# Kernel optimization log

Hardware: AMD Instinct MI355X
Metric: run time of the kernel (lower is better)

## Reference

```python
import jax, jax.numpy as jnp
import numpy as np

B = 16384          # scenes (batch_size)
K = 16             # vehicles per scene (1 hero + 15 neighbors)
IN_LEN = 16        # in_length
OUT_LEN = 25       # out_length
ALL_LEN = 41       # all_length
T_H = IN_LEN - 1
ENC = 64           # encoder_size
N = B * K
NN = B * (K - 1)


def setup_inputs() -> dict:
    key = jax.random.key(0)
    ks = jax.random.split(key, 20)
    scene = jax.random.normal(ks[0], (N, 2, ALL_LEN), jnp.float32)
    idx = jnp.arange(N, dtype=jnp.int32)
    hero_index = idx[::K]                 # hero is first vehicle of each group
    nbr_index = idx[idx % K != 0]         # remaining K-1 vehicles, group-major
    w = lambda k, s: jax.random.normal(k, s, jnp.float32) * 0.1
    return {
        'scene': scene, 'hero_index': hero_index, 'nbr_index': nbr_index,
        'W_h1': w(ks[1], (2 * IN_LEN, 32)), 'b_h1': w(ks[2], (32,)),
        'W_h2': w(ks[3], (32, ENC)), 'b_h2': w(ks[4], (ENC,)),
        'W_f1': w(ks[5], (2 * OUT_LEN, 32)), 'b_f1': w(ks[6], (32,)),
        'W_f2': w(ks[7], (32, ENC)), 'b_f2': w(ks[8], (ENC,)),
        'W_dyn': w(ks[9], (ENC, 32)), 'b_dyn': w(ks[10], (32,)),
        'W_nbr': w(ks[11], (2 * IN_LEN, ENC)), 'b_nbr': w(ks[12], (ENC,)),
        'W_out': w(ks[13], (96, 128)), 'b_out': w(ks[14], (128,)),
        'W_op': w(ks[15], (128, 1)), 'b_op': w(ks[16], (1,)),
    }


def reference(scene, hero_index, nbr_index,
              W_h1, b_h1, W_h2, b_h2, W_f1, b_f1, W_f2, b_f2,
              W_dyn, b_dyn, W_nbr, b_nbr, W_out, b_out, W_op, b_op):
    lrelu = lambda x: jax.nn.leaky_relu(x, 0.1)
    # per-scene reference pose = hero position at t_h, broadcast to all vehicles
    ref = scene[hero_index, :, T_H][:, :, None]              # (B,2,1)
    scene = scene - jnp.repeat(ref, K, axis=0)               # (N,2,ALL_LEN)
    # per-scene, per-channel scale = max |history| over vehicles and time
    scale = jnp.abs(scene[:, :, :IN_LEN]).reshape(B, K, 2, IN_LEN).max(axis=(1, 3))  # (B,2)
    scene = scene / jnp.repeat(scale, K, axis=0)[:, :, None]
    hero = scene[hero_index]                                 # (B,2,ALL_LEN)
    nbrs = scene[nbr_index]                                  # (NN,2,ALL_LEN)
    hist = hero[:, :, :IN_LEN].transpose(0, 2, 1)            # (B,IN_LEN,2)
    fut = hero[:, :, IN_LEN:IN_LEN + OUT_LEN].transpose(0, 2, 1)  # (B,OUT_LEN,2)
    nb_hist = nbrs[:, :, :IN_LEN].transpose(0, 2, 1)         # (NN,IN_LEN,2)
    rel = jnp.repeat(hist, K - 1, axis=0) - nb_hist          # (NN,IN_LEN,2)
    hist_f = hist.reshape(B, 2 * IN_LEN)
    fut_f = fut.reshape(B, 2 * OUT_LEN)
    rel_f = rel.reshape(NN, 2 * IN_LEN)
    # hero history encoder (mlp_net) + dyn_emb
    hist_enc = lrelu(lrelu(hist_f @ W_h1 + b_h1) @ W_h2 + b_h2)
    hist_enc = lrelu(hist_enc @ W_dyn + b_dyn)
    # neighbor relative encoder + per-scene max pool + dyn_emb
    rela_enc = lrelu(rel_f @ W_nbr + b_nbr)                  # (NN,ENC)
    pooled = rela_enc.reshape(B, K - 1, ENC).max(axis=1)     # (B,ENC)
    pooled = lrelu(pooled @ W_dyn + b_dyn)
    # future encoder (mlp_net_fut) + dyn_emb
    fut_enc = lrelu(lrelu(fut_f @ W_f1 + b_f1) @ W_f2 + b_f2)
    fut_enc = lrelu(fut_enc @ W_dyn + b_dyn)
    enc = jnp.concatenate([hist_enc, pooled, fut_enc], axis=1)  # (B,96)
    feature_enc = lrelu(enc @ W_out + b_out)                 # (B,128)
    logit = jax.nn.sigmoid(feature_enc @ W_op + b_op)        # (B,1)
    return logit, feature_enc
```

## Files before the change

kernel.cpp:

```cpp
#include <hip/hip_runtime.h>
#include <hip/hip_bf16.h>
#include <math.h>

#define NB 16384

typedef short short8 __attribute__((ext_vector_type(8)));
typedef float f32x4 __attribute__((ext_vector_type(4)));

__device__ __forceinline__ float lrelu(float x){ return x > 0.f ? x : 0.1f*x; }

__device__ __forceinline__ unsigned short f2b(float f){
  unsigned u = __builtin_bit_cast(unsigned, f);
  u = (u + 0x7fffu + ((u >> 16) & 1u)) >> 16;
  return (unsigned short)u;
}

#define MFMA(a,b,c) __builtin_amdgcn_mfma_f32_16x16x32_bf16((a),(b),(c),0,0,0)

__device__ __forceinline__ short8 afrag(const unsigned short* tile, int stride_us, int kbase){
  const int l = threadIdx.x & 63;
  return *(const short8*)(tile + (size_t)(l & 15) * stride_us + kbase + ((l >> 4) * 8));
}

__device__ __forceinline__ short8 ldfrag(const unsigned short* __restrict__ frags, int slot, int idx){
  return *(const short8*)(frags + ((size_t)((slot * 8 + idx) * 64 + (threadIdx.x & 63)) * 8));
}

__global__ __launch_bounds__(64) void prep_frags(
    const float* __restrict__ W_h1, const float* __restrict__ W_f1,
    const float* __restrict__ W_h2, const float* __restrict__ W_f2,
    const float* __restrict__ W_dyn, const float* __restrict__ W_nbr,
    const float* __restrict__ W_out, unsigned short* __restrict__ frags)
{
  const int bid = blockIdx.x;
  const int slot = bid >> 3, w = bid & 7;
  const int l = threadIdx.x;
  const int n16 = l & 15, q = l >> 4;
  short8 r = {0,0,0,0,0,0,0,0};
  #pragma unroll
  for (int e = 0; e < 8; ++e){
    const int p = q * 8 + e;
    int i = -1, n = -1, ldn = 0;
    const float* W = nullptr;
    switch (slot){
      case 0:  W = W_nbr; ldn = 64;  n = (w & 3) * 16 + n16; i = 2*(p&15) + (p>>4); break;
      case 1:  W = W_h1;  ldn = 32;  n = (w & 1) * 16 + n16; i = 2*(p&15) + (p>>4); break;
      case 2:  W = W_f1;  ldn = 32;  n = (w & 1) * 16 + n16; i = (p < 25) ? 2*p   : -1; break;
      case 3:  W = W_f1;  ldn = 32;  n = (w & 1) * 16 + n16; i = (p < 25) ? 2*p+1 : -1; break;
      case 4:  W = W_dyn; ldn = 32;  n = (w & 1) * 16 + n16; i = p;      break;
      case 5:  W = W_dyn; ldn = 32;  n = (w & 1) * 16 + n16; i = 32 + p; break;
      case 6:  W = W_h2;  ldn = 64;  n = (w & 3) * 16 + n16; i = p; break;
      case 7:  W = W_f2;  ldn = 64;  n = (w & 3) * 16 + n16; i = p; break;
      case 8:  W = W_out; ldn = 128; n = w * 16 + n16;       i = p;      break;
      case 9:  W = W_out; ldn = 128; n = w * 16 + n16;       i = 32 + p; break;
      case 10: W = W_out; ldn = 128; n = w * 16 + n16;       i = 64 + p; break;
    }
    const float v = (W && i >= 0) ? W[i * ldn + n] : 0.f;
    r[e] = (short)f2b(v);
  }
  *(short8*)(frags + (size_t)(bid * 64 + l) * 8) = r;
}

__global__ __launch_bounds__(512) void highway_fused(
    const float* __restrict__ scene,
    const unsigned short* __restrict__ frags,
    const float* __restrict__ b_h1, const float* __restrict__ b_h2,
    const float* __restrict__ b_f1, const float* __restrict__ b_f2,
    const float* __restrict__ b_dyn, const float* __restrict__ b_nbr,
    const float* __restrict__ b_out, const float* __restrict__ W_op,
    const float* __restrict__ b_op,
    float* __restrict__ logit, float* __restrict__ feat)
{
  __shared__ __align__(16) unsigned short An[15 * 648];
  __shared__ __align__(16) unsigned short Ah[16][40];
  __shared__ __align__(16) unsigned short Af[16][72];
  __shared__ __align__(16) unsigned short Apool[16][72];
  __shared__ __align__(16) unsigned short As1h[16][40];
  __shared__ __align__(16) unsigned short As1f[16][40];
  __shared__ __align__(16) unsigned short As2h[16][72];
  __shared__ __align__(16) unsigned short As2f[16][72];
  __shared__ __align__(16) unsigned short Aenc[16][104];
  __shared__ float tmpP[4][16][17];
  __shared__ float red[8][16];

  const int tid = threadIdx.x;
  const int w = tid >> 6, l = tid & 63;
  const int g0 = blockIdx.x * 16;

  {
    const int g = tid >> 5, s = tid & 31;
    const int c = s >> 4, t = s & 15;
    const float* sc = scene + (size_t)(g0 + g) * 1312;

    float v[16];
    #pragma unroll
    for (int k = 0; k < 16; ++k) v[k] = sc[k * 82 + c * 41 + t];
    const float vf0 = sc[c * 41 + 16 + t];
    const float vf1 = (t < 9) ? sc[c * 41 + 32 + t] : 0.f;

    const float ref = __shfl(v[0], (l & 32) | (c << 4) | 15, 64);

    float m = 0.f;
    #pragma unroll
    for (int k = 0; k < 16; ++k) m = fmaxf(m, fabsf(v[k] - ref));
    m = fmaxf(m, __shfl_xor(m, 1, 64));
    m = fmaxf(m, __shfl_xor(m, 2, 64));
    m = fmaxf(m, __shfl_xor(m, 4, 64));
    m = fmaxf(m, __shfl_xor(m, 8, 64));
    const float inv = 1.f / m;

    Ah[g][c * 16 + t] = f2b((v[0] - ref) * inv);
    #pragma unroll
    for (int j = 0; j < 15; ++j)
      An[j * 648 + g * 40 + c * 16 + t] = f2b((v[0] - v[j + 1]) * inv);
    Af[g][c * 32 + t] = f2b((vf0 - ref) * inv);
    Af[g][c * 32 + 16 + t] = (t < 9) ? f2b((vf1 - ref) * inv) : (unsigned short)0;
  }
  __syncthreads();

  f32x4 pm = {-1e30f,-1e30f,-1e30f,-1e30f};
  {
    const short8 wn = ldfrag(frags, 0, w);
    const int jbase = (w >> 2) ? 8 : 0;
    const int njt   = (w >> 2) ? 7 : 8;
    const float bn = b_nbr[(w & 3) * 16 + (l & 15)];
    for (int jj = 0; jj < njt; ++jj){
      const short8 a = afrag(An + (jbase + jj) * 648, 40, 0);
      f32x4 acc = {0.f,0.f,0.f,0.f};
      acc = MFMA(a, wn, acc);
      #pragma unroll
      for (int r = 0; r < 4; ++r) pm[r] = fmaxf(pm[r], lrelu(acc[r] + bn));
    }
    if (w >= 4){
      #pragma unroll
      for (int r = 0; r < 4; ++r) tmpP[w & 3][(l>>4)*4+r][l & 15] = pm[r];
    } else if (w < 2){
      const short8 a = afrag(&Ah[0][0], 40, 0);
      f32x4 acc = {0.f,0.f,0.f,0.f};
      acc = MFMA(a, ldfrag(frags, 1, w), acc);
      const float bb = b_h1[(w&1)*16 + (l&15)];
      #pragma unroll
      for (int r = 0; r < 4; ++r)
        As1h[(l>>4)*4+r][(w&1)*16+(l&15)] = f2b(lrelu(acc[r] + bb));
    } else {
      const short8 a0 = afrag(&Af[0][0], 72, 0);
      const short8 a1 = afrag(&Af[0][0], 72, 32);
      f32x4 acc = {0.f,0.f,0.f,0.f};
      acc = MFMA(a0, ldfrag(frags, 2, w), acc);
      acc = MFMA(a1, ldfrag(frags, 3, w), acc);
      const float bb = b_f1[(w&1)*16 + (l&15)];
      #pragma unroll
      for (int r = 0; r < 4; ++r)
        As1f[(l>>4)*4+r][(w&1)*16+(l&15)] = f2b(lrelu(acc[r] + bb));
    }
  }
  __syncthreads();

  if (w < 4){
    #pragma unroll
    for (int r = 0; r < 4; ++r){
      const float q = fmaxf(pm[r], tmpP[w & 3][(l>>4)*4+r][l & 15]);
      Apool[(l>>4)*4+r][(w&3)*16+(l&15)] = f2b(q);
    }
  } else {
    const short8 a = afrag(&As1h[0][0], 40, 0);
    f32x4 acc = {0.f,0.f,0.f,0.f};
    acc = MFMA(a, ldfrag(frags, 6, w), acc);
    const float bb = b_h2[(w&3)*16 + (l&15)];
    #pragma unroll
    for (int r = 0; r < 4; ++r)
      As2h[(l>>4)*4+r][(w&3)*16+(l&15)] = f2b(lrelu(acc[r] + bb));
  }
  __syncthreads();

  if (w < 4){
    const short8 a = afrag(&As1f[0][0], 40, 0);
    f32x4 acc = {0.f,0.f,0.f,0.f};
    acc = MFMA(a, ldfrag(frags, 7, w), acc);
    const float bb = b_f2[(w&3)*16 + (l&15)];
    #pragma unroll
    for (int r = 0; r < 4; ++r)
      As2f[(l>>4)*4+r][(w&3)*16+(l&15)] = f2b(lrelu(acc[r] + bb));
  } else {
    const unsigned short* src = (w < 6) ? &Apool[0][0] : &As2h[0][0];
    const int base = (w < 6) ? 32 : 0;
    const short8 a0 = afrag(src, 72, 0);
    const short8 a1 = afrag(src, 72, 32);
    f32x4 acc = {0.f,0.f,0.f,0.f};
    acc = MFMA(a0, ldfrag(frags, 4, w), acc);
    acc = MFMA(a1, ldfrag(frags, 5, w), acc);
    const float bb = b_dyn[(w&1)*16 + (l&15)];
    #pragma unroll
    for (int r = 0; r < 4; ++r)
      Aenc[(l>>4)*4+r][base+(w&1)*16+(l&15)] = f2b(lrelu(acc[r] + bb));
  }
  __syncthreads();

  if (w < 2){
    const short8 a0 = afrag(&As2f[0][0], 72, 0);
    const short8 a1 = afrag(&As2f[0][0], 72, 32);
    f32x4 acc = {0.f,0.f,0.f,0.f};
    acc = MFMA(a0, ldfrag(frags, 4, w), acc);
    acc = MFMA(a1, ldfrag(frags, 5, w), acc);
    const float bb = b_dyn[(w&1)*16 + (l&15)];
    #pragma unroll
    for (int r = 0; r < 4; ++r)
      Aenc[(l>>4)*4+r][64+(w&1)*16+(l&15)] = f2b(lrelu(acc[r] + bb));
  }
  __syncthreads();

  {
    const short8 a0 = afrag(&Aenc[0][0], 104, 0);
    const short8 a1 = afrag(&Aenc[0][0], 104, 32);
    const short8 a2 = afrag(&Aenc[0][0], 104, 64);
    f32x4 acc = {0.f,0.f,0.f,0.f};
    acc = MFMA(a0, ldfrag(frags, 8, w), acc);
    acc = MFMA(a1, ldfrag(frags, 9, w), acc);
    acc = MFMA(a2, ldfrag(frags, 10, w), acc);
    const float bb = b_out[w*16 + (l&15)];
    const float wop = W_op[w*16 + (l&15)];
    float p[4];
    #pragma unroll
    for (int r = 0; r < 4; ++r){
      const int gg = (l>>4)*4 + r;
      const float fe = lrelu(acc[r] + bb);
      feat[(size_t)(g0 + gg) * 128 + w*16 + (l&15)] = fe;
      p[r] = fe * wop;
    }
    #pragma unroll
    for (int r = 0; r < 4; ++r){
      p[r] += __shfl_xor(p[r], 1, 64);
      p[r] += __shfl_xor(p[r], 2, 64);
      p[r] += __shfl_xor(p[r], 4, 64);
      p[r] += __shfl_xor(p[r], 8, 64);
    }
    if ((l & 15) == 0){
      #pragma unroll
      for (int r = 0; r < 4; ++r) red[w][(l>>4)*4 + r] = p[r];
    }
  }
  __syncthreads();

  if (tid < 16){
    float sacc = b_op[0];
    #pragma unroll
    for (int ww = 0; ww < 8; ++ww) sacc += red[ww][tid];
    logit[g0 + tid] = 1.f / (1.f + expf(-sacc));
  }
}

extern "C" void kernel_launch(void* const* d_in, const int* in_sizes, int n_in,
                              void* d_out, int out_size, void* d_ws, size_t ws_size,
                              hipStream_t stream)
{
  (void)in_sizes; (void)n_in; (void)out_size; (void)ws_size;
  const float* scene = (const float*)d_in[0];
  const float* W_h1  = (const float*)d_in[3];
  const float* b_h1  = (const float*)d_in[4];
  const float* W_h2  = (const float*)d_in[5];
  const float* b_h2  = (const float*)d_in[6];
  const float* W_f1  = (const float*)d_in[7];
  const float* b_f1  = (const float*)d_in[8];
  const float* W_f2  = (const float*)d_in[9];
  const float* b_f2  = (const float*)d_in[10];
  const float* W_dyn = (const float*)d_in[11];
  const float* b_dyn = (const float*)d_in[12];
  const float* W_nbr = (const float*)d_in[13];
  const float* b_nbr = (const float*)d_in[14];
  const float* W_out = (const float*)d_in[15];
  const float* b_out = (const float*)d_in[16];
  const float* W_op  = (const float*)d_in[17];
  const float* b_op  = (const float*)d_in[18];

  unsigned short* frags = (unsigned short*)d_ws;

  float* logit = (float*)d_out;
  float* feat  = logit + NB;

  prep_frags<<<88, 64, 0, stream>>>(W_h1, W_f1, W_h2, W_f2, W_dyn, W_nbr, W_out, frags);
  highway_fused<<<NB / 16, 512, 0, stream>>>(scene, frags,
      b_h1, b_h2, b_f1, b_f2, b_dyn, b_nbr, b_out, W_op, b_op, logit, feat);
}
```

Measured before the change: 29.17 us.

## Halve scenes per block, pack two neighbor slots per MFMA tile, alias LDS

Each block now handles 8 scenes with 256 threads instead of 16 scenes with 512. The neighbor encoder packs two neighbor indices into one 16-row MFMA tile, so each wave covers all neighbors for its output columns and max-pools across lane halves with a shuffle, which removes the cross-wave tmpP buffer and one barrier. Shared-memory buffers are aliased into a single array to shrink LDS per block, the stage schedule is reshuffled to use five barriers instead of six, and the feature output uses nontemporal stores. In exchange, half of every MFMA row block is wasted in the later per-scene layers because only 8 rows are valid.

```diff
diff --git a/kernel.cpp b/kernel.cpp
--- a/kernel.cpp
+++ b/kernel.cpp
@@ -1,5 +1,4 @@
 #include <hip/hip_runtime.h>
-#include <hip/hip_bf16.h>
 #include <math.h>
 
 #define NB 16384
@@ -61,7 +60,7 @@
   *(short8*)(frags + (size_t)(bid * 64 + l) * 8) = r;
 }
 
-__global__ __launch_bounds__(512) void highway_fused(
+__global__ __launch_bounds__(256) void highway_fused(
     const float* __restrict__ scene,
     const unsigned short* __restrict__ frags,
     const float* __restrict__ b_h1, const float* __restrict__ b_h2,
@@ -71,21 +70,22 @@
     const float* __restrict__ b_op,
     float* __restrict__ logit, float* __restrict__ feat)
 {
-  __shared__ __align__(16) unsigned short An[15 * 648];
-  __shared__ __align__(16) unsigned short Ah[16][40];
-  __shared__ __align__(16) unsigned short Af[16][72];
-  __shared__ __align__(16) unsigned short Apool[16][72];
-  __shared__ __align__(16) unsigned short As1h[16][40];
-  __shared__ __align__(16) unsigned short As1f[16][40];
-  __shared__ __align__(16) unsigned short As2h[16][72];
-  __shared__ __align__(16) unsigned short As2f[16][72];
-  __shared__ __align__(16) unsigned short Aenc[16][104];
-  __shared__ float tmpP[4][16][17];
-  __shared__ float red[8][16];
+  __shared__ __align__(16) unsigned short S[9408];
+  __shared__ float red[4][8];
+  unsigned short* An    = S;
+  unsigned short* Ah    = S + 5184;
+  unsigned short* Af    = S + 5824;
+  unsigned short* As2h  = S;
+  unsigned short* As2f  = S + 1152;
+  unsigned short* Aenc  = S + 2304;
+  unsigned short* As1h  = S + 6976;
+  unsigned short* As1f  = S + 7616;
+  unsigned short* Apool = S + 8256;
 
   const int tid = threadIdx.x;
   const int w = tid >> 6, l = tid & 63;
-  const int g0 = blockIdx.x * 16;
+  const int col = l & 15;
+  const int g0 = blockIdx.x * 8;
 
   {
     const int g = tid >> 5, s = tid & 31;
@@ -109,142 +109,157 @@
     m = fmaxf(m, __shfl_xor(m, 8, 64));
     const float inv = 1.f / m;
 
-    Ah[g][c * 16 + t] = f2b((v[0] - ref) * inv);
-    #pragma unroll
-    for (int j = 0; j < 15; ++j)
-      An[j * 648 + g * 40 + c * 16 + t] = f2b((v[0] - v[j + 1]) * inv);
-    Af[g][c * 32 + t] = f2b((vf0 - ref) * inv);
-    Af[g][c * 32 + 16 + t] = (t < 9) ? f2b((vf1 - ref) * inv) : (unsigned short)0;
-  }
-  __syncthreads();
-
-  f32x4 pm = {-1e30f,-1e30f,-1e30f,-1e30f};
+    Ah[g * 40 + c * 16 + t] = f2b((v[0] - ref) * inv);
+    #pragma unroll
+    for (int j = 1; j < 16; ++j)
+      An[((j - 1) >> 1) * 648 + (((j - 1) & 1) * 8 + g) * 40 + c * 16 + t]
+        = f2b((v[0] - v[j]) * inv);
+    Af[g * 72 + c * 32 + t] = f2b((vf0 - ref) * inv);
+    Af[g * 72 + c * 32 + 16 + t] = (t < 9) ? f2b((vf1 - ref) * inv) : (unsigned short)0;
+    An[7 * 648 + (8 + (tid >> 5)) * 40 + (tid & 31)] = 0;
+  }
+  __syncthreads();
+
   {
     const short8 wn = ldfrag(frags, 0, w);
-    const int jbase = (w >> 2) ? 8 : 0;
-    const int njt   = (w >> 2) ? 7 : 8;
-    const float bn = b_nbr[(w & 3) * 16 + (l & 15)];
-    for (int jj = 0; jj < njt; ++jj){
-      const short8 a = afrag(An + (jbase + jj) * 648, 40, 0);
-      f32x4 acc = {0.f,0.f,0.f,0.f};
+    const float bn = b_nbr[w * 16 + col];
+    f32x4 pm = {-1e30f, -1e30f, -1e30f, -1e30f};
+    #pragma unroll
+    for (int jp = 0; jp < 8; ++jp){
+      const short8 a = afrag(An + jp * 648, 40, 0);
+      f32x4 acc = {0.f, 0.f, 0.f, 0.f};
       acc = MFMA(a, wn, acc);
-      #pragma unroll
-      for (int r = 0; r < 4; ++r) pm[r] = fmaxf(pm[r], lrelu(acc[r] + bn));
-    }
-    if (w >= 4){
-      #pragma unroll
-      for (int r = 0; r < 4; ++r) tmpP[w & 3][(l>>4)*4+r][l & 15] = pm[r];
-    } else if (w < 2){
-      const short8 a = afrag(&Ah[0][0], 40, 0);
-      f32x4 acc = {0.f,0.f,0.f,0.f};
+      if (jp < 7 || l < 32){
+        #pragma unroll
+        for (int r = 0; r < 4; ++r) pm[r] = fmaxf(pm[r], lrelu(acc[r] + bn));
+      }
+    }
+    #pragma unroll
+    for (int r = 0; r < 4; ++r) pm[r] = fmaxf(pm[r], __shfl_xor(pm[r], 32, 64));
+    if (l < 32){
+      #pragma unroll
+      for (int r = 0; r < 4; ++r)
+        Apool[((l >> 4) * 4 + r) * 72 + w * 16 + col] = f2b(pm[r]);
+    }
+
+    if (w < 2){
+      const short8 a = afrag(Ah, 40, 0);
+      f32x4 acc = {0.f, 0.f, 0.f, 0.f};
       acc = MFMA(a, ldfrag(frags, 1, w), acc);
-      const float bb = b_h1[(w&1)*16 + (l&15)];
-      #pragma unroll
-      for (int r = 0; r < 4; ++r)
-        As1h[(l>>4)*4+r][(w&1)*16+(l&15)] = f2b(lrelu(acc[r] + bb));
+      const float bb = b_h1[w * 16 + col];
+      #pragma unroll
+      for (int r = 0; r < 4; ++r)
+        As1h[((l >> 4) * 4 + r) * 40 + w * 16 + col] = f2b(lrelu(acc[r] + bb));
     } else {
-      const short8 a0 = afrag(&Af[0][0], 72, 0);
-      const short8 a1 = afrag(&Af[0][0], 72, 32);
-      f32x4 acc = {0.f,0.f,0.f,0.f};
-      acc = MFMA(a0, ldfrag(frags, 2, w), acc);
-      acc = MFMA(a1, ldfrag(frags, 3, w), acc);
-      const float bb = b_f1[(w&1)*16 + (l&15)];
-      #pragma unroll
-      for (int r = 0; r < 4; ++r)
-        As1f[(l>>4)*4+r][(w&1)*16+(l&15)] = f2b(lrelu(acc[r] + bb));
-    }
-  }
-  __syncthreads();
-
-  if (w < 4){
-    #pragma unroll
-    for (int r = 0; r < 4; ++r){
-      const float q = fmaxf(pm[r], tmpP[w & 3][(l>>4)*4+r][l & 15]);
-      Apool[(l>>4)*4+r][(w&3)*16+(l&15)] = f2b(q);
-    }
+      const int ct = w - 2;
+      const short8 a0 = afrag(Af, 72, 0);
+      const short8 a1 = afrag(Af, 72, 32);
+      f32x4 acc = {0.f, 0.f, 0.f, 0.f};
+      acc = MFMA(a0, ldfrag(frags, 2, ct), acc);
+      acc = MFMA(a1, ldfrag(frags, 3, ct), acc);
+      const float bb = b_f1[ct * 16 + col];
+      #pragma unroll
+      for (int r = 0; r < 4; ++r)
+        As1f[((l >> 4) * 4 + r) * 40 + ct * 16 + col] = f2b(lrelu(acc[r] + bb));
+    }
+  }
+  __syncthreads();
+
+  if (w < 2){
+    const short8 a0 = afrag(Apool, 72, 0);
+    const short8 a1 = afrag(Apool, 72, 32);
+    f32x4 acc = {0.f, 0.f, 0.f, 0.f};
+    acc = MFMA(a0, ldfrag(frags, 4, w), acc);
+    acc = MFMA(a1, ldfrag(frags, 5, w), acc);
+    const float bd = b_dyn[w * 16 + col];
+    #pragma unroll
+    for (int r = 0; r < 4; ++r)
+      Aenc[((l >> 4) * 4 + r) * 104 + 32 + w * 16 + col] = f2b(lrelu(acc[r] + bd));
+    const short8 a = afrag(As1h, 40, 0);
+    f32x4 acc2 = {0.f, 0.f, 0.f, 0.f};
+    acc2 = MFMA(a, ldfrag(frags, 6, w), acc2);
+    const float bh = b_h2[w * 16 + col];
+    #pragma unroll
+    for (int r = 0; r < 4; ++r)
+      As2h[((l >> 4) * 4 + r) * 72 + w * 16 + col] = f2b(lrelu(acc2[r] + bh));
   } else {
-    const short8 a = afrag(&As1h[0][0], 40, 0);
-    f32x4 acc = {0.f,0.f,0.f,0.f};
+    const short8 a = afrag(As1h, 40, 0);
+    f32x4 acc = {0.f, 0.f, 0.f, 0.f};
     acc = MFMA(a, ldfrag(frags, 6, w), acc);
-    const float bb = b_h2[(w&3)*16 + (l&15)];
-    #pragma unroll
-    for (int r = 0; r < 4; ++r)
-      As2h[(l>>4)*4+r][(w&3)*16+(l&15)] = f2b(lrelu(acc[r] + bb));
-  }
-  __syncthreads();
-
-  if (w < 4){
-    const short8 a = afrag(&As1f[0][0], 40, 0);
-    f32x4 acc = {0.f,0.f,0.f,0.f};
-    acc = MFMA(a, ldfrag(frags, 7, w), acc);
-    const float bb = b_f2[(w&3)*16 + (l&15)];
-    #pragma unroll
-    for (int r = 0; r < 4; ++r)
-      As2f[(l>>4)*4+r][(w&3)*16+(l&15)] = f2b(lrelu(acc[r] + bb));
-  } else {
-    const unsigned short* src = (w < 6) ? &Apool[0][0] : &As2h[0][0];
-    const int base = (w < 6) ? 32 : 0;
+    const float bh = b_h2[w * 16 + col];
+    #pragma unroll
+    for (int r = 0; r < 4; ++r)
+      As2h[((l >> 4) * 4 + r) * 72 + w * 16 + col] = f2b(lrelu(acc[r] + bh));
+    const short8 af_ = afrag(As1f, 40, 0);
+    #pragma unroll
+    for (int u = 0; u < 2; ++u){
+      const int ct = (w - 2) * 2 + u;
+      f32x4 acc2 = {0.f, 0.f, 0.f, 0.f};
+      acc2 = MFMA(af_, ldfrag(frags, 7, ct), acc2);
+      const float bf = b_f2[ct * 16 + col];
+      #pragma unroll
+      for (int r = 0; r < 4; ++r)
+        As2f[((l >> 4) * 4 + r) * 72 + ct * 16 + col] = f2b(lrelu(acc2[r] + bf));
+    }
+  }
+  __syncthreads();
+
+  {
+    const unsigned short* src = (w < 2) ? As2h : As2f;
+    const int ct = w & 1;
+    const int base = (w < 2) ? 0 : 64;
     const short8 a0 = afrag(src, 72, 0);
     const short8 a1 = afrag(src, 72, 32);
-    f32x4 acc = {0.f,0.f,0.f,0.f};
-    acc = MFMA(a0, ldfrag(frags, 4, w), acc);
-    acc = MFMA(a1, ldfrag(frags, 5, w), acc);
-    const float bb = b_dyn[(w&1)*16 + (l&15)];
-    #pragma unroll
-    for (int r = 0; r < 4; ++r)
-      Aenc[(l>>4)*4+r][base+(w&1)*16+(l&15)] = f2b(lrelu(acc[r] + bb));
-  }
-  __syncthreads();
-
-  if (w < 2){
-    const short8 a0 = afrag(&As2f[0][0], 72, 0);
-    const short8 a1 = afrag(&As2f[0][0], 72, 32);
-    f32x4 acc = {0.f,0.f,0.f,0.f};
-    acc = MFMA(a0, ldfrag(frags, 4, w), acc);
-    acc = MFMA(a1, ldfrag(frags, 5, w), acc);
-    const float bb = b_dyn[(w&1)*16 + (l&15)];
-    #pragma unroll
-    for (int r = 0; r < 4; ++r)
-      Aenc[(l>>4)*4+r][64+(w&1)*16+(l&15)] = f2b(lrelu(acc[r] + bb));
-  }
-  __syncthreads();
-
-  {
-    const short8 a0 = afrag(&Aenc[0][0], 104, 0);
-    const short8 a1 = afrag(&Aenc[0][0], 104, 32);
-    const short8 a2 = afrag(&Aenc[0][0], 104, 64);
-    f32x4 acc = {0.f,0.f,0.f,0.f};
-    acc = MFMA(a0, ldfrag(frags, 8, w), acc);
-    acc = MFMA(a1, ldfrag(frags, 9, w), acc);
-    acc = MFMA(a2, ldfrag(frags, 10, w), acc);
-    const float bb = b_out[w*16 + (l&15)];
-    const float wop = W_op[w*16 + (l&15)];
-    float p[4];
+    f32x4 acc = {0.f, 0.f, 0.f, 0.f};
+    acc = MFMA(a0, ldfrag(frags, 4, ct), acc);
+    acc = MFMA(a1, ldfrag(frags, 5, ct), acc);
+    const float bd = b_dyn[ct * 16 + col];
+    #pragma unroll
+    for (int r = 0; r < 4; ++r)
+      Aenc[((l >> 4) * 4 + r) * 104 + base + ct * 16 + col] = f2b(lrelu(acc[r] + bd));
+  }
+  __syncthreads();
+
+  {
+    const short8 a0 = afrag(Aenc, 104, 0);
+    const short8 a1 = afrag(Aenc, 104, 32);
+    const short8 a2 = afrag(Aenc, 104, 64);
+    float psum[4] = {0.f, 0.f, 0.f, 0.f};
+    #pragma unroll
+    for (int u = 0; u < 2; ++u){
+      const int ct = 2 * w + u;
+      f32x4 acc = {0.f, 0.f, 0.f, 0.f};
+      acc = MFMA(a0, ldfrag(frags, 8, ct), acc);
+      acc = MFMA(a1, ldfrag(frags, 9, ct), acc);
+      acc = MFMA(a2, ldfrag(frags, 10, ct), acc);
+      const float bb = b_out[ct * 16 + col];
+      const float wop = W_op[ct * 16 + col];
+      if (l < 32){
+        #pragma unroll
+        for (int r = 0; r < 4; ++r){
+          const int gg = (l >> 4) * 4 + r;
+          const float fe = lrelu(acc[r] + bb);
+          __builtin_nontemporal_store(fe, &feat[(size_t)(g0 + gg) * 128 + ct * 16 + col]);
+          psum[r] += fe * wop;
+        }
+      }
+    }
     #pragma unroll
     for (int r = 0; r < 4; ++r){
-      const int gg = (l>>4)*4 + r;
-      const float fe = lrelu(acc[r] + bb);
-      feat[(size_t)(g0 + gg) * 128 + w*16 + (l&15)] = fe;
-      p[r] = fe * wop;
-    }
-    #pragma unroll
-    for (int r = 0; r < 4; ++r){
-      p[r] += __shfl_xor(p[r], 1, 64);
-      p[r] += __shfl_xor(p[r], 2, 64);
-      p[r] += __shfl_xor(p[r], 4, 64);
-      p[r] += __shfl_xor(p[r], 8, 64);
-    }
-    if ((l & 15) == 0){
-      #pragma unroll
-      for (int r = 0; r < 4; ++r) red[w][(l>>4)*4 + r] = p[r];
-    }
-  }
-  __syncthreads();
-
-  if (tid < 16){
-    float sacc = b_op[0];
-    #pragma unroll
-    for (int ww = 0; ww < 8; ++ww) sacc += red[ww][tid];
+      psum[r] += __shfl_xor(psum[r], 1, 64);
+      psum[r] += __shfl_xor(psum[r], 2, 64);
+      psum[r] += __shfl_xor(psum[r], 4, 64);
+      psum[r] += __shfl_xor(psum[r], 8, 64);
+    }
+    if (col == 0 && l < 32){
+      #pragma unroll
+      for (int r = 0; r < 4; ++r) red[w][(l >> 4) * 4 + r] = psum[r];
+    }
+  }
+  __syncthreads();
+
+  if (tid < 8){
+    const float sacc = b_op[0] + red[0][tid] + red[1][tid] + red[2][tid] + red[3][tid];
     logit[g0 + tid] = 1.f / (1.f + expf(-sacc));
   }
 }
@@ -278,6 +293,6 @@
   float* feat  = logit + NB;
 
   prep_frags<<<88, 64, 0, stream>>>(W_h1, W_f1, W_h2, W_f2, W_dyn, W_nbr, W_out, frags);
-  highway_fused<<<NB / 16, 512, 0, stream>>>(scene, frags,
+  highway_fused<<<NB / 8, 256, 0, stream>>>(scene, frags,
       b_h1, b_h2, b_f1, b_f2, b_dyn, b_nbr, b_out, W_op, b_op, logit, feat);
 }
```

Result: slower. 29.78 us (+2.1%).
